# Optimization experiments

Measured on AMD Instinct MI355X. Metric: run time of the kernel, lower is better.

Reference implementation:

```python
import jax, jax.numpy as jnp
import numpy as np

B, D_IN, H, OUT = 4096, 2048, 4096, 1000
TEMPERATURE = 0.5


def _l2_normalize(w):
    return w / jnp.linalg.norm(w, axis=1, keepdims=True)


def setup_inputs() -> dict:
    key = jax.random.key(0)
    ks = jax.random.split(key, 8)
    x = jax.random.normal(ks[0], (B, D_IN), dtype=jnp.float32)
    kohonen_weights = _l2_normalize(jax.random.normal(ks[1], (H, D_IN), dtype=jnp.float32))
    # MLP: 4096 -> 2048 -> 1024 -> 1000 (hidden_layers=2, div=2)
    def lin(k, fan_in, fan_out):
        kw, kb = jax.random.split(k)
        bound = 1.0 / np.sqrt(fan_in)
        W = jax.random.uniform(kw, (fan_out, fan_in), minval=-bound, maxval=bound, dtype=jnp.float32)
        b = jax.random.uniform(kb, (fan_out,), minval=-bound, maxval=bound, dtype=jnp.float32)
        return W, b
    w1, b1 = lin(ks[2], H, H // 2)
    w2, b2 = lin(ks[3], H // 2, H // 4)
    w3, b3 = lin(ks[4], H // 4, OUT)
    return {"x": x, "kohonen_weights": kohonen_weights,
            "w1": w1, "b1": b1, "w2": w2, "b2": b2, "w3": w3, "b3": b3}


def reference(x, kohonen_weights, w1, b1, w2, b2, w3, b3):
    # pairwise euclidean distances [B, H] via expanded GEMM (cdist p=2)
    x2 = jnp.sum(x * x, axis=1, keepdims=True)            # [B,1]
    w2sq = jnp.sum(kohonen_weights * kohonen_weights, axis=1)  # [H]
    d2 = x2 + w2sq[None, :] - 2.0 * (x @ kohonen_weights.T)
    distances = jnp.sqrt(jnp.maximum(d2, 1e-12))
    winners = jnp.argmin(distances, axis=1)
    soft = jax.nn.softmax(-distances / TEMPERATURE, axis=1)
    # MLP (dropout=0 / eval mode)
    h = jax.nn.relu(soft @ w1.T + b1)
    h = jax.nn.relu(h @ w2.T + b2)
    output = h @ w3.T + b3
    return output, winners
```

## Files before the change

### kernel.cpp

```cpp
#include <hip/hip_runtime.h>
#include <hip/hip_bf16.h>
#include <stdint.h>

typedef __attribute__((ext_vector_type(4))) float f32x4;
typedef __attribute__((ext_vector_type(8))) __bf16 bf16x8;
typedef unsigned short u16;
typedef unsigned long long u64;

__device__ __forceinline__ u16 f2bf(float f){
  unsigned u = __float_as_uint(f);
  u += 0x7fffu + ((u >> 16) & 1u);
  return (u16)(u >> 16);
}

__device__ __forceinline__ void gload16(const u16* g, u16* l){
  __builtin_amdgcn_global_load_lds(
      (__attribute__((address_space(1))) void*)g,
      (__attribute__((address_space(3))) void*)l, 16, 0, 0);
}

__global__ __launch_bounds__(64)
void cvt_rows(const float* __restrict__ src, u16* __restrict__ dst,
              float* __restrict__ sq)
{
#pragma clang fp contract(off)
  const int row = blockIdx.x;
  const int l = threadIdx.x;
  const float* r = src + (size_t)row * 2048;
  const f32x4* r4 = (const f32x4*)r;
  ushort4* d4 = (ushort4*)(dst + (size_t)row * 2048);
#pragma unroll
  for (int i = 0; i < 8; i++){
    f32x4 v = r4[l + 64*i];
    ushort4 o;
    o.x = f2bf(v.x); o.y = f2bf(v.y); o.z = f2bf(v.z); o.w = f2bf(v.w);
    d4[l + 64*i] = o;
  }
  float leaf = 0.f;
  if (l < 16){
    const float* p = r + l*128;
    float rr[8];
#pragma unroll
    for (int j = 0; j < 8; j++){ float v = p[j]; rr[j] = v*v; }
    for (int i = 8; i < 128; i += 8){
#pragma unroll
      for (int j = 0; j < 8; j++){ float v = p[i+j]; float vv = v*v; rr[j] = rr[j] + vv; }
    }
    leaf = ((rr[0]+rr[1])+(rr[2]+rr[3]))+((rr[4]+rr[5])+(rr[6]+rr[7]));
  }
#pragma unroll
  for (int s = 1; s < 16; s <<= 1){
    float o = __shfl_down(leaf, s);
    if ((l & (2*s - 1)) == 0) leaf = leaf + o;
  }
  if (l == 0) sq[row] = leaf;
}

__global__ __launch_bounds__(256)
void cvt_mat(const float* __restrict__ src, u16* __restrict__ dst, int n4)
{
  const f32x4* s4 = (const f32x4*)src;
  ushort4* d4 = (ushort4*)dst;
  for (int i = blockIdx.x*256 + threadIdx.x; i < n4; i += gridDim.x*256){
    f32x4 v = s4[i];
    ushort4 o;
    o.x = f2bf(v.x); o.y = f2bf(v.y); o.z = f2bf(v.z); o.w = f2bf(v.w);
    d4[i] = o;
  }
}

template<int BM, int BN, int WM, int WN, int EPI>
__global__ __launch_bounds__(WM*WN*64, 2)
void gemm_p(const u16* __restrict__ A, const u16* __restrict__ Bm,
            float* __restrict__ Cf, u16* __restrict__ Cb,
            const float* __restrict__ bias,
            int M, int N, int K, int ncols, int nbn)
{
  constexpr int T  = WM*WN*64;
  constexpr int FM = BM/(WM*16);
  constexpr int FN = BN/(WN*16);
  constexpr int ABYTES = BM*64;
  constexpr int BUFB   = (BM+BN)*64;
  constexpr int RA = ABYTES/(T*16);
  constexpr int RB = (BN*64)/(T*16);
  extern __shared__ char lds[];

  const int t = threadIdx.x;
  const int nwg = gridDim.x;
  const int cpx = nwg >> 3;
  const int bid = blockIdx.x;
  const int wg  = (bid & 7)*cpx + (bid >> 3);
  const int bm = wg / nbn, bn = wg % nbn;
  const int brow = bm*BM, bcol = bn*BN;

  const int l = t & 63, w = t >> 6;
  const int wm = w / WN, wn = w % WN;
  const int wr = wm*(FM*16), wc = wn*(FN*16);
  const int fr = l & 15, fk = (l >> 4)*8;
  const int xk = fk ^ ((fr & 12) << 1);

  const int srow = t >> 2;
  const int scol = (t & 3)*8;

  const u16* agp[RA]; const u16* bgp[RB];
#pragma unroll
  for (int r = 0; r < RA; r++){
    const int row = r*(T>>2) + srow;
    agp[r] = A + (size_t)(brow + row)*K + (scol ^ ((row & 12) << 1));
  }
#pragma unroll
  for (int r = 0; r < RB; r++){
    const int row = r*(T>>2) + srow;
    bgp[r] = Bm + (size_t)(bcol + row)*K + (scol ^ ((row & 12) << 1));
  }

  f32x4 acc[FM][FN] = {};
  const int nt = K >> 5;

  auto stageA = [&](int kt, int buf){
    char* dst = lds + buf*BUFB + t*16;
#pragma unroll
    for (int r = 0; r < RA; r++)
      gload16(agp[r] + (kt << 5), (u16*)(dst + r*T*16));
  };
  auto stageB = [&](int kt, int buf){
    char* dst = lds + buf*BUFB + ABYTES + t*16;
#pragma unroll
    for (int r = 0; r < RB; r++)
      gload16(bgp[r] + (kt << 5), (u16*)(dst + r*T*16));
  };

  stageA(0, 0); stageB(0, 0);
  stageA(1, 1); stageB(1, 1);
  asm volatile("s_waitcnt vmcnt(4)" ::: "memory");
  __builtin_amdgcn_s_barrier();

  for (int kt = 0; kt < nt; kt++){
    const int buf = kt % 3;
    const u16* As = (const u16*)(lds + buf*BUFB);
    const u16* Bs = (const u16*)(lds + buf*BUFB + ABYTES);
    const bool pre = (kt + 2 < nt);
    const int nbuf = (kt + 2) % 3;

    bf16x8 av[FM], bv[FN];
#pragma unroll
    for (int m = 0; m < FM; m++)
      av[m] = *(const bf16x8*)(As + (wr + m*16 + fr)*32 + xk);
#pragma unroll
    for (int n = 0; n < FN/2; n++)
      bv[n] = *(const bf16x8*)(Bs + (wc + n*16 + fr)*32 + xk);
    if (pre) stageA(kt + 2, nbuf);
    __builtin_amdgcn_s_barrier();
    __builtin_amdgcn_s_setprio(1);
#pragma unroll
    for (int m = 0; m < FM; m++)
#pragma unroll
      for (int n = 0; n < FN/2; n++)
        acc[m][n] = __builtin_amdgcn_mfma_f32_16x16x32_bf16(av[m], bv[n], acc[m][n], 0, 0, 0);
    __builtin_amdgcn_s_setprio(0);

#pragma unroll
    for (int n = FN/2; n < FN; n++)
      bv[n] = *(const bf16x8*)(Bs + (wc + n*16 + fr)*32 + xk);
    if (pre) stageB(kt + 2, nbuf);
    __builtin_amdgcn_s_barrier();
    __builtin_amdgcn_s_setprio(1);
#pragma unroll
    for (int m = 0; m < FM; m++)
#pragma unroll
      for (int n = FN/2; n < FN; n++)
        acc[m][n] = __builtin_amdgcn_mfma_f32_16x16x32_bf16(av[m], bv[n], acc[m][n], 0, 0, 0);
    __builtin_amdgcn_s_setprio(0);

    if (kt + 1 < nt){
      if (pre) asm volatile("s_waitcnt vmcnt(4)" ::: "memory");
      else     asm volatile("s_waitcnt vmcnt(0)" ::: "memory");
      __builtin_amdgcn_s_barrier();
    }
  }

#pragma unroll
  for (int n = 0; n < FN; n++){
    const int gcol = bcol + wc + n*16 + fr;
    float bvv = 0.f;
    if (EPI == 1) bvv = bias[gcol];
    if (EPI == 2 && gcol < ncols) bvv = bias[gcol];
#pragma unroll
    for (int m = 0; m < FM; m++){
      const int grow = brow + wr + m*16 + (l >> 4)*4;
#pragma unroll
      for (int r = 0; r < 4; r++){
        float v = acc[m][n][r];
        if (EPI == 0){
          Cf[(size_t)(grow + r)*N + gcol] = v;
        } else if (EPI == 1){
          Cb[(size_t)(grow + r)*N + gcol] = f2bf(fmaxf(v + bvv, 0.f));
        } else {
          if (gcol < ncols) Cf[(size_t)(grow + r)*ncols + gcol] = v + bvv;
        }
      }
    }
  }
}

__global__ __launch_bounds__(256)
void row_softmax(const float* __restrict__ S, const float* __restrict__ x2,
                 const float* __restrict__ w2sq,
                 const float* __restrict__ x, const float* __restrict__ W,
                 u16* __restrict__ soft, float* __restrict__ winners)
{
  const int b = blockIdx.x, t = threadIdx.x;
  const float x2b = x2[b];
  const f32x4* S4 = (const f32x4*)(S + (size_t)b*4096);
  const f32x4* W24 = (const f32x4*)w2sq;
  float dv[16];
  float bd = 3.0e38f; int bc = 0;
#pragma unroll
  for (int i = 0; i < 4; i++){
    f32x4 s = S4[t + 256*i];
    f32x4 wv = W24[t + 256*i];
#pragma unroll
    for (int j = 0; j < 4; j++){
      float u = x2b + wv[j];
      float d2 = u - 2.0f*s[j];
      float d = __fsqrt_rn(fmaxf(d2, 1e-12f));
      dv[i*4 + j] = d;
      if (d < bd){ bd = d; bc = (t + 256*i)*4 + j; }
    }
  }
  u64 key = ((u64)__float_as_uint(bd) << 32) | (unsigned)bc;
#pragma unroll
  for (int s = 1; s < 64; s <<= 1){
    u64 o = __shfl_xor(key, s);
    if (o < key) key = o;
  }
  __shared__ u64 wk[4];
  __shared__ double csum[4];
  __shared__ float fred[4];
  __shared__ int ccnt;
  __shared__ int cand[32];
  if ((t & 63) == 0) wk[t >> 6] = key;
  if (t == 0) ccnt = 0;
  __syncthreads();
  u64 k0 = wk[0];
  if (wk[1] < k0) k0 = wk[1];
  if (wk[2] < k0) k0 = wk[2];
  if (wk[3] < k0) k0 = wk[3];
  const float dmin = __uint_as_float((unsigned)(k0 >> 32));

  const float thr = dmin + 0.01f;
#pragma unroll
  for (int i = 0; i < 4; i++)
#pragma unroll
    for (int j = 0; j < 4; j++)
      if (dv[i*4 + j] <= thr){
        int p = atomicAdd(&ccnt, 1);
        if (p < 32) cand[p] = (t + 256*i)*4 + j;
      }
  __syncthreads();
  const int nc = min(ccnt, 32);

  float bestd = 3.0e38f; int besti = 0x7fffffff;
  const f32x4* xp = (const f32x4*)(x + (size_t)b*2048) + t*2;
  f32x4 xv0 = xp[0], xv1 = xp[1];
  for (int c = 0; c < nc; c++){
    const int h = cand[c];
    const f32x4* wp = (const f32x4*)(W + (size_t)h*2048) + t*2;
    f32x4 wv0 = wp[0], wv1 = wp[1];
    double a = 0.0;
#pragma unroll
    for (int j = 0; j < 4; j++) a += (double)xv0[j]*(double)wv0[j];
#pragma unroll
    for (int j = 0; j < 4; j++) a += (double)xv1[j]*(double)wv1[j];
#pragma unroll
    for (int s = 1; s < 64; s <<= 1) a += __shfl_xor(a, s);
    if ((t & 63) == 0) csum[t >> 6] = a;
    __syncthreads();
    if (t == 0){
      double tt = (csum[0] + csum[1]) + (csum[2] + csum[3]);
      float t32 = (float)tt;
      float u = x2b + w2sq[h];
      float d2 = u - 2.0f*t32;
      float d = __fsqrt_rn(fmaxf(d2, 1e-12f));
      if (d < bestd || (d == bestd && h < besti)){ bestd = d; besti = h; }
    }
    __syncthreads();
  }
  if (t == 0) winners[b] = (float)besti;

  float es = 0.f;
#pragma unroll
  for (int i = 0; i < 16; i++) es += __expf(-2.0f*(dv[i] - dmin));
#pragma unroll
  for (int s = 1; s < 64; s <<= 1) es += __shfl_xor(es, s);
  if ((t & 63) == 0) fred[t >> 6] = es;
  __syncthreads();
  const float tot = (fred[0] + fred[1]) + (fred[2] + fred[3]);
  const float inv = 1.0f / tot;
  ushort4* o4 = (ushort4*)(soft + (size_t)b*4096);
#pragma unroll
  for (int i = 0; i < 4; i++){
    ushort4 o;
    o.x = f2bf(__expf(-2.0f*(dv[i*4+0] - dmin))*inv);
    o.y = f2bf(__expf(-2.0f*(dv[i*4+1] - dmin))*inv);
    o.z = f2bf(__expf(-2.0f*(dv[i*4+2] - dmin))*inv);
    o.w = f2bf(__expf(-2.0f*(dv[i*4+3] - dmin))*inv);
    o4[t + 256*i] = o;
  }
}

extern "C" void kernel_launch(void* const* d_in, const int* in_sizes, int n_in,
                              void* d_out, int out_size, void* d_ws, size_t ws_size,
                              hipStream_t stream)
{
  const float* x  = (const float*)d_in[0];
  const float* Wk = (const float*)d_in[1];
  const float* w1 = (const float*)d_in[2];
  const float* b1 = (const float*)d_in[3];
  const float* w2 = (const float*)d_in[4];
  const float* b2 = (const float*)d_in[5];
  const float* w3 = (const float*)d_in[6];
  const float* b3 = (const float*)d_in[7];
  float* out = (float*)d_out;
  float* winners = out + (size_t)4096*1000;

  char* ws = (char*)d_ws;
  const size_t MB = 1u << 20;
  float* S   = (float*)(ws);
  u16* xb    = (u16*)(ws + 64*MB);
  u16* wb    = (u16*)(ws + 80*MB);
  u16* soft  = (u16*)(ws + 64*MB);
  u16* w1b   = (u16*)(ws + 96*MB);
  u16* w2b   = (u16*)(ws + 112*MB);
  u16* w3b   = (u16*)(ws + 116*MB);
  float* x2  = (float*)(ws + 118*MB);
  float* w2s = x2 + 4096;
  u16* h1    = (u16*)(ws);
  u16* h2    = (u16*)(ws + 16*MB);

  cvt_rows<<<4096, 64, 0, stream>>>(x, xb, x2);
  cvt_rows<<<4096, 64, 0, stream>>>(Wk, wb, w2s);
  cvt_mat<<<2048, 256, 0, stream>>>(w1, w1b, 2048*4096/4);
  cvt_mat<<<1024, 256, 0, stream>>>(w2, w2b, 1024*2048/4);
  hipMemsetAsync(w3b, 0, (size_t)1024*1024*2, stream);
  cvt_mat<<<512, 256, 0, stream>>>(w3, w3b, 1000*1024/4);

  hipFuncSetAttribute((const void*)gemm_p<256,256,2,4,0>,
                      hipFuncAttributeMaxDynamicSharedMemorySize, 3*512*64);
  gemm_p<256,256,2,4,0><<<256, 512, 3*512*64, stream>>>(
      xb, wb, S, nullptr, nullptr, 4096, 4096, 2048, 0, 16);

  row_softmax<<<4096, 256, 0, stream>>>(S, x2, w2s, x, Wk, soft, winners);

  gemm_p<128,128,2,2,1><<<512, 256, 3*256*64, stream>>>(
      soft, w1b, nullptr, h1, b1, 4096, 2048, 4096, 0, 16);
  gemm_p<128,128,2,2,1><<<256, 256, 3*256*64, stream>>>(
      h1, w2b, nullptr, h2, b2, 4096, 1024, 2048, 0, 8);
  gemm_p<128,128,2,2,2><<<256, 256, 3*256*64, stream>>>(
      h2, w3b, out, nullptr, b3, 4096, 1024, 1024, 1000, 8);
}
```

Measured before the change: 288.2 us.

## Store distance GEMM output as bf16, retile MLP GEMMs, change LDS swizzle

The distance GEMM now writes its dot products as bf16 instead of fp32, and the softmax kernel reads them back as bf16. This halves the traffic of the 4096x4096 intermediate. The first MLP GEMM moves to 256x128 tiles with 512 threads, the smaller GEMMs get a min-waves launch bound of 3, and the LDS XOR swizzle pattern changes. The norm reduction is vectorised and the single-phase MFMA schedule is used for small tiles. Rounding the dot products to bf16 before subtracting from the norms can cause large relative error in d2 and may flip argmin winners.

```diff
diff --git a/kernel.cpp b/kernel.cpp
--- a/kernel.cpp
+++ b/kernel.cpp
@@ -12,11 +12,22 @@
   u += 0x7fffu + ((u >> 16) & 1u);
   return (u16)(u >> 16);
 }
+__device__ __forceinline__ float bf2f(u16 v){
+  return __uint_as_float(((unsigned)v) << 16);
+}
 
 __device__ __forceinline__ void gload16(const u16* g, u16* l){
   __builtin_amdgcn_global_load_lds(
       (__attribute__((address_space(1))) void*)g,
       (__attribute__((address_space(3))) void*)l, 16, 0, 0);
+}
+
+template<int N> __device__ __forceinline__ void waitcnt_vm(){
+  if constexpr (N==0) asm volatile("s_waitcnt vmcnt(0)" ::: "memory");
+  else if constexpr (N==2) asm volatile("s_waitcnt vmcnt(2)" ::: "memory");
+  else if constexpr (N==3) asm volatile("s_waitcnt vmcnt(3)" ::: "memory");
+  else if constexpr (N==4) asm volatile("s_waitcnt vmcnt(4)" ::: "memory");
+  else if constexpr (N==6) asm volatile("s_waitcnt vmcnt(6)" ::: "memory");
 }
 
 __global__ __launch_bounds__(64)
@@ -38,15 +49,15 @@
   }
   float leaf = 0.f;
   if (l < 16){
-    const float* p = r + l*128;
-    float rr[8];
-#pragma unroll
-    for (int j = 0; j < 8; j++){ float v = p[j]; rr[j] = v*v; }
-    for (int i = 8; i < 128; i += 8){
-#pragma unroll
-      for (int j = 0; j < 8; j++){ float v = p[i+j]; float vv = v*v; rr[j] = rr[j] + vv; }
-    }
-    leaf = ((rr[0]+rr[1])+(rr[2]+rr[3]))+((rr[4]+rr[5])+(rr[6]+rr[7]));
+    const f32x4* p4 = (const f32x4*)(r + l*128);
+    f32x4 a0 = {0.f,0.f,0.f,0.f}, a1 = {0.f,0.f,0.f,0.f};
+#pragma unroll
+    for (int i = 0; i < 32; i += 2){
+      f32x4 v0 = p4[i], v1 = p4[i+1];
+      a0 = a0 + v0*v0;
+      a1 = a1 + v1*v1;
+    }
+    leaf = ((a0.x+a0.y)+(a0.z+a0.w))+((a1.x+a1.y)+(a1.z+a1.w));
   }
 #pragma unroll
   for (int s = 1; s < 16; s <<= 1){
@@ -69,8 +80,8 @@
   }
 }
 
-template<int BM, int BN, int WM, int WN, int EPI>
-__global__ __launch_bounds__(WM*WN*64, 2)
+template<int BM, int BN, int WM, int WN, int EPI, int MINW>
+__global__ __launch_bounds__(WM*WN*64, MINW)
 void gemm_p(const u16* __restrict__ A, const u16* __restrict__ Bm,
             float* __restrict__ Cf, u16* __restrict__ Cb,
             const float* __restrict__ bias,
@@ -83,6 +94,8 @@
   constexpr int BUFB   = (BM+BN)*64;
   constexpr int RA = ABYTES/(T*16);
   constexpr int RB = (BN*64)/(T*16);
+  constexpr int IF = RA + RB;
+  constexpr int NPH = (FM*FN >= 32) ? 2 : 1;
   extern __shared__ char lds[];
 
   const int t = threadIdx.x;
@@ -97,22 +110,18 @@
   const int wm = w / WN, wn = w % WN;
   const int wr = wm*(FM*16), wc = wn*(FN*16);
   const int fr = l & 15, fk = (l >> 4)*8;
-  const int xk = fk ^ ((fr & 12) << 1);
+  const int xk = fk ^ (((fr >> 1) & 3) << 3);
 
   const int srow = t >> 2;
-  const int scol = (t & 3)*8;
+  const int scol = ((t & 3)*8) ^ (((t >> 3) & 3) << 3);
 
   const u16* agp[RA]; const u16* bgp[RB];
 #pragma unroll
-  for (int r = 0; r < RA; r++){
-    const int row = r*(T>>2) + srow;
-    agp[r] = A + (size_t)(brow + row)*K + (scol ^ ((row & 12) << 1));
-  }
-#pragma unroll
-  for (int r = 0; r < RB; r++){
-    const int row = r*(T>>2) + srow;
-    bgp[r] = Bm + (size_t)(bcol + row)*K + (scol ^ ((row & 12) << 1));
-  }
+  for (int r = 0; r < RA; r++)
+    agp[r] = A + (size_t)(brow + r*(T>>2) + srow)*K + scol;
+#pragma unroll
+  for (int r = 0; r < RB; r++)
+    bgp[r] = Bm + (size_t)(bcol + r*(T>>2) + srow)*K + scol;
 
   f32x4 acc[FM][FN] = {};
   const int nt = K >> 5;
@@ -132,7 +141,7 @@
 
   stageA(0, 0); stageB(0, 0);
   stageA(1, 1); stageB(1, 1);
-  asm volatile("s_waitcnt vmcnt(4)" ::: "memory");
+  waitcnt_vm<IF>();
   __builtin_amdgcn_s_barrier();
 
   for (int kt = 0; kt < nt; kt++){
@@ -146,35 +155,51 @@
 #pragma unroll
     for (int m = 0; m < FM; m++)
       av[m] = *(const bf16x8*)(As + (wr + m*16 + fr)*32 + xk);
-#pragma unroll
-    for (int n = 0; n < FN/2; n++)
-      bv[n] = *(const bf16x8*)(Bs + (wc + n*16 + fr)*32 + xk);
-    if (pre) stageA(kt + 2, nbuf);
-    __builtin_amdgcn_s_barrier();
-    __builtin_amdgcn_s_setprio(1);
-#pragma unroll
-    for (int m = 0; m < FM; m++)
+
+    if (NPH == 1){
+#pragma unroll
+      for (int n = 0; n < FN; n++)
+        bv[n] = *(const bf16x8*)(Bs + (wc + n*16 + fr)*32 + xk);
+      if (pre){ stageA(kt + 2, nbuf); stageB(kt + 2, nbuf); }
+      __builtin_amdgcn_s_barrier();
+      __builtin_amdgcn_s_setprio(1);
+#pragma unroll
+      for (int m = 0; m < FM; m++)
+#pragma unroll
+        for (int n = 0; n < FN; n++)
+          acc[m][n] = __builtin_amdgcn_mfma_f32_16x16x32_bf16(av[m], bv[n], acc[m][n], 0, 0, 0);
+      __builtin_amdgcn_s_setprio(0);
+    } else {
 #pragma unroll
       for (int n = 0; n < FN/2; n++)
-        acc[m][n] = __builtin_amdgcn_mfma_f32_16x16x32_bf16(av[m], bv[n], acc[m][n], 0, 0, 0);
-    __builtin_amdgcn_s_setprio(0);
-
-#pragma unroll
-    for (int n = FN/2; n < FN; n++)
-      bv[n] = *(const bf16x8*)(Bs + (wc + n*16 + fr)*32 + xk);
-    if (pre) stageB(kt + 2, nbuf);
-    __builtin_amdgcn_s_barrier();
-    __builtin_amdgcn_s_setprio(1);
-#pragma unroll
-    for (int m = 0; m < FM; m++)
+        bv[n] = *(const bf16x8*)(Bs + (wc + n*16 + fr)*32 + xk);
+      if (pre) stageA(kt + 2, nbuf);
+      __builtin_amdgcn_s_barrier();
+      __builtin_amdgcn_s_setprio(1);
+#pragma unroll
+      for (int m = 0; m < FM; m++)
+#pragma unroll
+        for (int n = 0; n < FN/2; n++)
+          acc[m][n] = __builtin_amdgcn_mfma_f32_16x16x32_bf16(av[m], bv[n], acc[m][n], 0, 0, 0);
+      __builtin_amdgcn_s_setprio(0);
+
 #pragma unroll
       for (int n = FN/2; n < FN; n++)
-        acc[m][n] = __builtin_amdgcn_mfma_f32_16x16x32_bf16(av[m], bv[n], acc[m][n], 0, 0, 0);
-    __builtin_amdgcn_s_setprio(0);
+        bv[n] = *(const bf16x8*)(Bs + (wc + n*16 + fr)*32 + xk);
+      if (pre) stageB(kt + 2, nbuf);
+      __builtin_amdgcn_s_barrier();
+      __builtin_amdgcn_s_setprio(1);
+#pragma unroll
+      for (int m = 0; m < FM; m++)
+#pragma unroll
+        for (int n = FN/2; n < FN; n++)
+          acc[m][n] = __builtin_amdgcn_mfma_f32_16x16x32_bf16(av[m], bv[n], acc[m][n], 0, 0, 0);
+      __builtin_amdgcn_s_setprio(0);
+    }
 
     if (kt + 1 < nt){
-      if (pre) asm volatile("s_waitcnt vmcnt(4)" ::: "memory");
-      else     asm volatile("s_waitcnt vmcnt(0)" ::: "memory");
+      if (pre) waitcnt_vm<IF>();
+      else     waitcnt_vm<0>();
       __builtin_amdgcn_s_barrier();
     }
   }
@@ -195,8 +220,10 @@
           Cf[(size_t)(grow + r)*N + gcol] = v;
         } else if (EPI == 1){
           Cb[(size_t)(grow + r)*N + gcol] = f2bf(fmaxf(v + bvv, 0.f));
+        } else if (EPI == 2){
+          if (gcol < ncols) Cf[(size_t)(grow + r)*ncols + gcol] = v + bvv;
         } else {
-          if (gcol < ncols) Cf[(size_t)(grow + r)*ncols + gcol] = v + bvv;
+          Cb[(size_t)(grow + r)*N + gcol] = f2bf(v);
         }
       }
     }
@@ -204,25 +231,26 @@
 }
 
 __global__ __launch_bounds__(256)
-void row_softmax(const float* __restrict__ S, const float* __restrict__ x2,
+void row_softmax(const u16* __restrict__ Sb, const float* __restrict__ x2,
                  const float* __restrict__ w2sq,
                  const float* __restrict__ x, const float* __restrict__ W,
                  u16* __restrict__ soft, float* __restrict__ winners)
 {
   const int b = blockIdx.x, t = threadIdx.x;
   const float x2b = x2[b];
-  const f32x4* S4 = (const f32x4*)(S + (size_t)b*4096);
+  const ushort4* S4 = (const ushort4*)(Sb + (size_t)b*4096);
   const f32x4* W24 = (const f32x4*)w2sq;
   float dv[16];
   float bd = 3.0e38f; int bc = 0;
 #pragma unroll
   for (int i = 0; i < 4; i++){
-    f32x4 s = S4[t + 256*i];
+    ushort4 s = S4[t + 256*i];
     f32x4 wv = W24[t + 256*i];
+    float sf[4] = {bf2f(s.x), bf2f(s.y), bf2f(s.z), bf2f(s.w)};
 #pragma unroll
     for (int j = 0; j < 4; j++){
       float u = x2b + wv[j];
-      float d2 = u - 2.0f*s[j];
+      float d2 = u - 2.0f*sf[j];
       float d = __fsqrt_rn(fmaxf(d2, 1e-12f));
       dv[i*4 + j] = d;
       if (d < bd){ bd = d; bc = (t + 256*i)*4 + j; }
@@ -326,14 +354,14 @@
 
   char* ws = (char*)d_ws;
   const size_t MB = 1u << 20;
-  float* S   = (float*)(ws);
-  u16* xb    = (u16*)(ws + 64*MB);
-  u16* wb    = (u16*)(ws + 80*MB);
-  u16* soft  = (u16*)(ws + 64*MB);
-  u16* w1b   = (u16*)(ws + 96*MB);
-  u16* w2b   = (u16*)(ws + 112*MB);
-  u16* w3b   = (u16*)(ws + 116*MB);
-  float* x2  = (float*)(ws + 118*MB);
+  u16* Sb    = (u16*)(ws);
+  u16* xb    = (u16*)(ws + 32*MB);
+  u16* wb    = (u16*)(ws + 48*MB);
+  u16* soft  = (u16*)(ws + 32*MB);
+  u16* w1b   = (u16*)(ws + 64*MB);
+  u16* w2b   = (u16*)(ws + 80*MB);
+  u16* w3b   = (u16*)(ws + 84*MB);
+  float* x2  = (float*)(ws + 86*MB);
   float* w2s = x2 + 4096;
   u16* h1    = (u16*)(ws);
   u16* h2    = (u16*)(ws + 16*MB);
@@ -345,17 +373,25 @@
   hipMemsetAsync(w3b, 0, (size_t)1024*1024*2, stream);
   cvt_mat<<<512, 256, 0, stream>>>(w3, w3b, 1000*1024/4);
 
-  hipFuncSetAttribute((const void*)gemm_p<256,256,2,4,0>,
+  hipFuncSetAttribute((const void*)gemm_p<256,256,2,4,3,2>,
                       hipFuncAttributeMaxDynamicSharedMemorySize, 3*512*64);
-  gemm_p<256,256,2,4,0><<<256, 512, 3*512*64, stream>>>(
-      xb, wb, S, nullptr, nullptr, 4096, 4096, 2048, 0, 16);
-
-  row_softmax<<<4096, 256, 0, stream>>>(S, x2, w2s, x, Wk, soft, winners);
-
-  gemm_p<128,128,2,2,1><<<512, 256, 3*256*64, stream>>>(
+  gemm_p<256,256,2,4,3,2><<<256, 512, 3*512*64, stream>>>(
+      xb, wb, nullptr, Sb, nullptr, 4096, 4096, 2048, 0, 16);
+
+  row_softmax<<<4096, 256, 0, stream>>>(Sb, x2, w2s, x, Wk, soft, winners);
+
+  hipFuncSetAttribute((const void*)gemm_p<256,128,4,2,1,2>,
+                      hipFuncAttributeMaxDynamicSharedMemorySize, 3*384*64);
+  gemm_p<256,128,4,2,1,2><<<256, 512, 3*384*64, stream>>>(
       soft, w1b, nullptr, h1, b1, 4096, 2048, 4096, 0, 16);
-  gemm_p<128,128,2,2,1><<<256, 256, 3*256*64, stream>>>(
+
+  hipFuncSetAttribute((const void*)gemm_p<128,128,2,2,1,3>,
+                      hipFuncAttributeMaxDynamicSharedMemorySize, 3*256*64);
+  gemm_p<128,128,2,2,1,3><<<256, 256, 3*256*64, stream>>>(
       h1, w2b, nullptr, h2, b2, 4096, 1024, 2048, 0, 8);
-  gemm_p<128,128,2,2,2><<<256, 256, 3*256*64, stream>>>(
+
+  hipFuncSetAttribute((const void*)gemm_p<128,128,2,2,2,3>,
+                      hipFuncAttributeMaxDynamicSharedMemorySize, 3*256*64);
+  gemm_p<128,128,2,2,2,3><<<256, 256, 3*256*64, stream>>>(
       h2, w3b, out, nullptr, b3, 4096, 1024, 1024, 1000, 8);
 }
```

After: 274.8 us. 4.7% less time.
